# Kernel optimization log

Hardware: AMD Instinct MI355X
Metric: run time of the kernel (lower is better)

Reference implementation:

```python
import jax, jax.numpy as jnp
import numpy as np

CONF_THRESH = 0.3
NMS_THRESH = 0.5
TOP_K = 64
VAR = (0.1, 0.2)  # standard SSD decode variances


def setup_inputs() -> dict:
    key = jax.random.key(0)
    k1, k2, k3 = jax.random.split(key, 3)
    B, A, C = 16, 16384, 81
    loc = jax.random.normal(k1, (B, A, 4), jnp.float32)
    conf = jax.random.normal(k2, (B, A, C), jnp.float32)
    anchors = jax.random.uniform(k3, (A, 4), jnp.float32)  # cxcywh in [0,1]
    return {"loc": loc, "conf": conf, "anchors": anchors}


def _decode(loc, anchors):
    # SSD-style decode: loc [A,4] offsets, anchors [A,4] cxcywh -> corners [A,4]
    cxcy = anchors[:, :2] + loc[:, :2] * VAR[0] * anchors[:, 2:]
    wh = anchors[:, 2:] * jnp.exp(loc[:, 2:] * VAR[1])
    tl = cxcy - wh * 0.5
    return jnp.concatenate([tl, tl + wh], axis=1)


def _iou(box, boxes):
    # box [4], boxes [A,4] in corner format
    tl = jnp.maximum(box[:2], boxes[:, :2])
    br = jnp.minimum(box[2:], boxes[:, 2:])
    wh = jnp.clip(br - tl, 0.0)
    inter = wh[:, 0] * wh[:, 1]
    a1 = (box[2] - box[0]) * (box[3] - box[1])
    a2 = (boxes[:, 2] - boxes[:, 0]) * (boxes[:, 3] - boxes[:, 1])
    return inter / (a1 + a2 - inter)


def _nms(boxes, scores):
    # greedy NMS for one (batch, class) lane; boxes [A,4], scores [A]
    s0 = jnp.where(scores > CONF_THRESH, scores, -1.0)

    def step(s, _):
        i = jnp.argmax(s)
        sc = s[i]
        box = boxes[i]
        keep = sc > 0.0  # -1 means masked/suppressed; valid scores > conf_thresh > 0
        supp = jnp.where(_iou(box, boxes) > NMS_THRESH, -1.0, s).at[i].set(-1.0)
        s_next = jnp.where(keep, supp, s)
        row = jnp.where(keep, jnp.concatenate([sc[None], box]),
                        jnp.zeros((5,), s.dtype))
        return s_next, row

    _, rows = jax.lax.scan(step, s0, None, length=TOP_K)
    return rows  # [TOP_K, 5] = (score, x1, y1, x2, y2), zero-padded


def reference(loc, conf, anchors):
    conf = jax.nn.sigmoid(conf)                      # [B,A,C]
    boxes = jax.vmap(_decode, in_axes=(0, None))(loc, anchors)  # [B,A,4]
    scores = jnp.swapaxes(conf, 1, 2)                # [B,C,A]
    per_class = jax.vmap(_nms, in_axes=(None, 0))    # over classes
    out = jax.vmap(per_class)(boxes, scores)         # [B,C,TOP_K,5]
    return out
```

## Files before the change

kernel.cpp:

```cpp
#include <hip/hip_runtime.h>
#include <math.h>

constexpr int B_N  = 16;
constexpr int A_N  = 16384;
constexpr int C_N  = 81;
constexpr int TOPK = 64;
constexpr int DNT  = 256;
constexpr int NBINS = 232;
constexpr int CAP   = 512;
constexpr unsigned BIN_BASE = 0x3E99u;
constexpr int SNT = 256;
constexpr int BC_N = B_N * C_N;

constexpr int TA   = 64;
constexpr int TNT  = 256;
constexpr int TILE_ELEMS = TA * C_N;
constexpr int TILE_F4    = TILE_ELEMS / 4;

__global__ __launch_bounds__(DNT) void decode_kernel(const float4* __restrict__ loc,
                                                     const float4* __restrict__ anch,
                                                     float4* __restrict__ boxes) {
    int i = blockIdx.x * DNT + threadIdx.x;
    int a = i & (A_N - 1);
    float4 l  = loc[i];
    float4 an = anch[a];
    float cx = an.x + (l.x * 0.1f) * an.z;
    float cy = an.y + (l.y * 0.1f) * an.w;
    float w  = an.z * expf(l.z * 0.2f);
    float h  = an.w * expf(l.w * 0.2f);
    float x1 = cx - w * 0.5f;
    float y1 = cy - h * 0.5f;
    boxes[i] = make_float4(x1, y1, x1 + w, y1 + h);
}

__global__ __launch_bounds__(TNT) void sigT_kernel(const float* __restrict__ conf,
                                                   float* __restrict__ scoresT) {
    __shared__ float4 tile4[TILE_F4];
    float* tile = (float*)tile4;

    const int a0 = blockIdx.x * TA;
    const int b  = blockIdx.y;
    const int t  = threadIdx.x;

    const float4* src = (const float4*)(conf + ((size_t)b * A_N + a0) * C_N);
#pragma unroll
    for (int i = 0; i < (TILE_F4 + TNT - 1) / TNT; ++i) {
        int idx4 = i * TNT + t;
        if (idx4 < TILE_F4) {
            float4 x = src[idx4];
            float4 v;
            v.x = 1.0f / (1.0f + expf(-x.x));
            v.y = 1.0f / (1.0f + expf(-x.y));
            v.z = 1.0f / (1.0f + expf(-x.z));
            v.w = 1.0f / (1.0f + expf(-x.w));
            tile4[idx4] = v;
        }
    }
    __syncthreads();
    float* dst = scoresT + (size_t)b * C_N * A_N + a0;
#pragma unroll
    for (int i = 0; i < (TILE_F4 + TNT - 1) / TNT; ++i) {
        int idx4 = i * TNT + t;
        if (idx4 < TILE_F4) {
            int cc  = idx4 >> 4;
            int al4 = idx4 & 15;
            int e   = al4 * 4 * C_N + cc;
            float4 v;
            v.x = tile[e];
            v.y = tile[e + C_N];
            v.z = tile[e + 2 * C_N];
            v.w = tile[e + 3 * C_N];
            ((float4*)(dst + (size_t)cc * A_N))[al4] = v;
        }
    }
}

__device__ __forceinline__ void sort_gather_scan64(
        unsigned long long* cand, float4* cbox, int C, int lane,
        const float4* __restrict__ bptr, float* __restrict__ optr,
        float& rx1, float& ry1, float& rx2, float& ry2, float& rar,
        int& acc, int& kout) {
    unsigned long long key[8];
#pragma unroll
    for (int r = 0; r < 8; ++r) {
        int sidx = r * 64 + lane;
        key[r] = (sidx < C) ? cand[sidx] : 0ull;
    }
#pragma unroll
    for (int k = 2; k <= CAP; k <<= 1) {
#pragma unroll
        for (int j = k >> 1; j > 0; j >>= 1) {
            if (j >= 64) {
                int jr = j >> 6;
#pragma unroll
                for (int r = 0; r < 8; ++r) {
                    int rp = r ^ jr;
                    if (rp > r) {
                        int e = r * 64 + lane;
                        bool up = ((e & k) == 0);
                        unsigned long long va = key[r], vb = key[rp];
                        bool sw = up ? (va < vb) : (va > vb);
                        if (sw) { key[r] = vb; key[rp] = va; }
                    }
                }
            } else {
#pragma unroll
                for (int r = 0; r < 8; ++r) {
                    int e = r * 64 + lane;
                    bool up    = ((e & k) == 0);
                    bool isLow = ((lane & j) == 0);
                    unsigned long long va = key[r];
                    unsigned long long vb = __shfl_xor(va, j, 64);
                    bool keepMax = (up == isLow);
                    key[r] = keepMax ? (va > vb ? va : vb) : (va < vb ? va : vb);
                }
            }
        }
    }
    __syncthreads();
#pragma unroll
    for (int r = 0; r < 8; ++r) cand[r * 64 + lane] = key[r];
    __syncthreads();
#pragma unroll
    for (int r = 0; r < 8; ++r) {
        int e = r * 64 + lane;
        if (e < C) cbox[e] = bptr[(int)(~(unsigned)cand[e])];
    }
    __syncthreads();

    int ts = 0;
    unsigned long long k0 = cand[0];
    float4 cb = cbox[0];
    while (ts < C) {
        unsigned long long nk = 0ull;
        float4 nb = cb;
        if (ts + 1 < C) { nk = cand[ts + 1]; nb = cbox[ts + 1]; }
        float sc = __uint_as_float((unsigned)(k0 >> 32));
        float ca = (cb.z - cb.x) * (cb.w - cb.y);
        bool over = false;
        if (lane < acc) {
            float tlx = fmaxf(rx1, cb.x);
            float tly = fmaxf(ry1, cb.y);
            float brx = fminf(rx2, cb.z);
            float bry = fminf(ry2, cb.w);
            float iw  = fmaxf(brx - tlx, 0.0f);
            float ih  = fmaxf(bry - tly, 0.0f);
            float inter = iw * ih;
            float iou = inter / (rar + ca - inter);
            over = iou > 0.5f;
        }
        if (!__any(over)) {
            if (lane == acc) { rx1 = cb.x; ry1 = cb.y; rx2 = cb.z; ry2 = cb.w; rar = ca; }
            if (lane == 0) {
                float* o = optr + (size_t)kout * 5;
                o[0] = sc; o[1] = cb.x; o[2] = cb.y; o[3] = cb.z; o[4] = cb.w;
            }
            acc++; kout++;
            if (acc == TOPK) break;
        }
        ++ts; k0 = nk; cb = nb;
    }
}

__device__ __forceinline__ void suppress_pass(
        unsigned& aliveM, const float4& bb, float bar,
        const float4 (&breg)[8], const float (&careg)[8]) {
#pragma unroll
    for (int r = 0; r < 8; ++r) {
        float tlx = fmaxf(bb.x, breg[r].x);
        float tly = fmaxf(bb.y, breg[r].y);
        float brx = fminf(bb.z, breg[r].z);
        float bry = fminf(bb.w, breg[r].w);
        float iw  = fmaxf(brx - tlx, 0.0f);
        float ih  = fmaxf(bry - tly, 0.0f);
        float inter = iw * ih;
        float iou = inter / (bar + careg[r] - inter);
        if (iou > 0.5f) aliveM &= ~(1u << r);
    }
}

__device__ __forceinline__ void process_band64(
        unsigned long long* cand, float4* cbox, float4* abox, float* aar,
        int C, int lane,
        const float4* __restrict__ bptr, float* __restrict__ optr,
        int& acc, int& kout) {
    unsigned long long key[8];
#pragma unroll
    for (int r = 0; r < 8; ++r) {
        int sidx = r * 64 + lane;
        key[r] = (sidx < C) ? cand[sidx] : 0ull;
    }
#pragma unroll
    for (int k = 2; k <= CAP; k <<= 1) {
#pragma unroll
        for (int j = k >> 1; j > 0; j >>= 1) {
            if (j >= 64) {
                int jr = j >> 6;
#pragma unroll
                for (int r = 0; r < 8; ++r) {
                    int rp = r ^ jr;
                    if (rp > r) {
                        int e = r * 64 + lane;
                        bool up = ((e & k) == 0);
                        unsigned long long va = key[r], vb = key[rp];
                        bool sw = up ? (va < vb) : (va > vb);
                        if (sw) { key[r] = vb; key[rp] = va; }
                    }
                }
            } else {
#pragma unroll
                for (int r = 0; r < 8; ++r) {
                    int e = r * 64 + lane;
                    bool up    = ((e & k) == 0);
                    bool isLow = ((lane & j) == 0);
                    unsigned long long va = key[r];
                    unsigned long long vb = __shfl_xor(va, j, 64);
                    bool keepMax = (up == isLow);
                    key[r] = keepMax ? (va > vb ? va : vb) : (va < vb ? va : vb);
                }
            }
        }
    }
    __syncthreads();
#pragma unroll
    for (int r = 0; r < 8; ++r) cand[r * 64 + lane] = key[r];
    __syncthreads();

    float4 breg[8];
    float  careg[8];
#pragma unroll
    for (int r = 0; r < 8; ++r) {
        int e = r * 64 + lane;
        float4 v = make_float4(0.f, 0.f, 0.f, 0.f);
        if (e < C) { v = bptr[(int)(~(unsigned)cand[e])]; cbox[e] = v; }
        breg[r]  = v;
        careg[r] = (v.z - v.x) * (v.w - v.y);
    }
    __syncthreads();

    unsigned aliveM = 0;
#pragma unroll
    for (int r = 0; r < 8; ++r)
        if (r * 64 + lane < C) aliveM |= (1u << r);

    for (int a = 0; a < acc; ++a) {
        float4 bb = abox[a];
        float bar = aar[a];
        suppress_pass(aliveM, bb, bar, breg, careg);
    }

    int rStart = 0;
    while (acc < TOPK) {
        int estar = -1;
        for (int r = rStart; r < 8; ++r) {
            unsigned long long m = __ballot((aliveM >> r) & 1);
            if (m != 0ull) { estar = r * 64 + __builtin_ctzll(m); rStart = r; break; }
        }
        if (estar < 0) break;

        unsigned long long k0 = cand[estar];
        float4 bb = cbox[estar];
        float sc  = __uint_as_float((unsigned)(k0 >> 32));
        float bar = (bb.z - bb.x) * (bb.w - bb.y);

        if (lane == 0) {
            float* o = optr + (size_t)kout * 5;
            o[0] = sc; o[1] = bb.x; o[2] = bb.y; o[3] = bb.z; o[4] = bb.w;
            abox[acc] = bb; aar[acc] = bar;
        }
        acc++; kout++;

        suppress_pass(aliveM, bb, bar, breg, careg);
    }
}

__global__ __launch_bounds__(SNT) void select_kernel(
        const float* __restrict__ scoresT,
        unsigned long long* __restrict__ g_cand,
        int* __restrict__ g_hist,
        int* __restrict__ g_cnt,
        int* __restrict__ g_blo) {
    __shared__ int hist[NBINS];
    __shared__ int s_cnt;

    const int bc = blockIdx.x;
    const int t  = threadIdx.x;

    for (int i = t; i < NBINS; i += SNT) hist[i] = 0;
    if (t == 0) s_cnt = 0;
    __syncthreads();

    const float4* sptr = (const float4*)(scoresT + (size_t)bc * A_N);

    for (int i = 0; i < A_N / 4 / SNT; ++i) {
        float4 s4 = sptr[t + SNT * i];
        float s[4] = {s4.x, s4.y, s4.z, s4.w};
#pragma unroll
        for (int q = 0; q < 4; ++q) {
            if (s[q] > 0.3f) {
                unsigned u = __float_as_uint(s[q]);
                int bin = (int)(u >> 16) - (int)BIN_BASE;
                bin = bin < 0 ? 0 : (bin > NBINS - 1 ? NBINS - 1 : bin);
                atomicAdd(&hist[bin], 1);
            }
        }
    }
    __syncthreads();

    for (int i = t; i < NBINS; i += SNT) g_hist[bc * NBINS + i] = hist[i];

    int lo = NBINS, tot = 0;
    while (lo > 0) {
        int cnt = hist[lo - 1];
        if (tot + cnt > CAP) {
            if (tot == 0) { lo--; }
            break;
        }
        tot += cnt; lo--;
    }
    const int bin_lo = lo;

    if (bin_lo < NBINS) {
        for (int i = 0; i < A_N / 4 / SNT; ++i) {
            float4 s4 = sptr[t + SNT * i];
            float s[4] = {s4.x, s4.y, s4.z, s4.w};
#pragma unroll
            for (int q = 0; q < 4; ++q) {
                if (s[q] > 0.3f) {
                    unsigned u = __float_as_uint(s[q]);
                    int bin = (int)(u >> 16) - (int)BIN_BASE;
                    bin = bin < 0 ? 0 : (bin > NBINS - 1 ? NBINS - 1 : bin);
                    if (bin >= bin_lo && bin < NBINS) {
                        int slot = atomicAdd(&s_cnt, 1);
                        if (slot < CAP) {
                            unsigned a = (unsigned)(4 * (t + SNT * i) + q);
                            g_cand[(size_t)bc * CAP + slot] =
                                ((unsigned long long)u << 32) | (unsigned)(~a);
                        }
                    }
                }
            }
        }
    }
    __syncthreads();
    if (t == 0) {
        int C = s_cnt; if (C > CAP) C = CAP;
        g_cnt[bc] = C;
        g_blo[bc] = bin_lo;
    }
}

__global__ __launch_bounds__(64, 2) void nms_sorted_kernel(
        const float* __restrict__ scoresT,
        const float4* __restrict__ boxes,
        const unsigned long long* __restrict__ g_cand,
        const int* __restrict__ g_hist,
        const int* __restrict__ g_cnt,
        const int* __restrict__ g_blo,
        float* __restrict__ out) {
    __shared__ int hist[NBINS];
    __shared__ unsigned long long cand[CAP];
    __shared__ float4 cbox[CAP];
    __shared__ float4 abox[TOPK];
    __shared__ float  aar[TOPK];
    __shared__ int s_cnt;

    const int bc   = blockIdx.x;
    const int b    = bc / C_N;
    const int lane = threadIdx.x;

    const float4* sptr = (const float4*)(scoresT + (size_t)bc * A_N);
    const float4* bptr = boxes + (size_t)b * A_N;
    float* optr = out + (size_t)bc * TOPK * 5;

    for (int i = lane; i < NBINS; i += 64) hist[i] = g_hist[bc * NBINS + i];
    const int C0 = g_cnt[bc];
    int bin_hi   = g_blo[bc];
    for (int e = lane; e < C0; e += 64) cand[e] = g_cand[(size_t)bc * CAP + e];
    __syncthreads();

    int acc = 0, kout = 0;

    if (C0 > 0)
        process_band64(cand, cbox, abox, aar, C0, lane, bptr, optr, acc, kout);

    while (acc < TOPK) {
        int lo = bin_hi, tot = 0;
        while (lo > 0) {
            int cnt = hist[lo - 1];
            if (tot + cnt > CAP) {
                if (tot == 0) { lo--; }
                break;
            }
            tot += cnt; lo--;
        }
        const int bin_lo = lo;
        if (bin_lo == bin_hi) break;
        if (lane == 0) s_cnt = 0;
        __syncthreads();

        for (int i = 0; i < A_N / 4 / 64; ++i) {
            float4 s4 = sptr[lane + 64 * i];
            float s[4] = {s4.x, s4.y, s4.z, s4.w};
#pragma unroll
            for (int q = 0; q < 4; ++q) {
                if (s[q] > 0.3f) {
                    unsigned u = __float_as_uint(s[q]);
                    int bin = (int)(u >> 16) - (int)BIN_BASE;
                    bin = bin < 0 ? 0 : (bin > NBINS - 1 ? NBINS - 1 : bin);
                    if (bin >= bin_lo && bin < bin_hi) {
                        int slot = atomicAdd(&s_cnt, 1);
                        if (slot < CAP) {
                            unsigned a = (unsigned)(4 * (lane + 64 * i) + q);
                            cand[slot] = ((unsigned long long)u << 32) | (unsigned)(~a);
                        }
                    }
                }
            }
        }
        __syncthreads();
        int C = s_cnt; if (C > CAP) C = CAP;
        if (C > 0)
            process_band64(cand, cbox, abox, aar, C, lane, bptr, optr, acc, kout);
        bin_hi = bin_lo;
    }

    {
        float* o  = optr + (size_t)kout * 5;
        int   rem = (TOPK - kout) * 5;
        for (int i = lane; i < rem; i += 64) o[i] = 0.0f;
    }
}

__global__ __launch_bounds__(SNT, 4) void select_nms_fused(
        const float* __restrict__ scoresT,
        const float4* __restrict__ boxes,
        float* __restrict__ out) {
    __shared__ int hist[NBINS];
    __shared__ unsigned long long cand[CAP];
    __shared__ float4 cbox[CAP];
    __shared__ int s_cnt, s_acc, s_kout;

    const int bc   = blockIdx.x;
    const int b    = bc / C_N;
    const int t    = threadIdx.x;
    const int lane = t & 63;
    const int wv   = t >> 6;

    for (int i = t; i < NBINS; i += SNT) hist[i] = 0;
    if (t == 0) { s_acc = 0; s_kout = 0; }
    __syncthreads();

    const float4* sptr = (const float4*)(scoresT + (size_t)bc * A_N);
    const float4* bptr = boxes + (size_t)b * A_N;
    float* optr = out + (size_t)bc * TOPK * 5;

    for (int i = 0; i < A_N / 4 / SNT; ++i) {
        float4 s4 = sptr[t + SNT * i];
        float s[4] = {s4.x, s4.y, s4.z, s4.w};
#pragma unroll
        for (int q = 0; q < 4; ++q) {
            if (s[q] > 0.3f) {
                unsigned u = __float_as_uint(s[q]);
                int bin = (int)(u >> 16) - (int)BIN_BASE;
                bin = bin < 0 ? 0 : (bin > NBINS - 1 ? NBINS - 1 : bin);
                atomicAdd(&hist[bin], 1);
            }
        }
    }
    __syncthreads();

    float rx1 = 0.f, ry1 = 0.f, rx2 = 0.f, ry2 = 0.f, rar = 0.f;
    int acc = 0, kout = 0;

    int bin_hi = NBINS;
    for (;;) {
        int lo = bin_hi, tot = 0;
        while (lo > 0) {
            int cnt = hist[lo - 1];
            if (tot + cnt > CAP) { if (tot == 0) { lo--; } break; }
            tot += cnt; lo--;
        }
        const int bin_lo = lo;
        if (bin_lo == bin_hi) break;
        if (t == 0) s_cnt = 0;
        __syncthreads();

        for (int i = 0; i < A_N / 4 / SNT; ++i) {
            float4 s4 = sptr[t + SNT * i];
            float s[4] = {s4.x, s4.y, s4.z, s4.w};
#pragma unroll
            for (int q = 0; q < 4; ++q) {
                if (s[q] > 0.3f) {
                    unsigned u = __float_as_uint(s[q]);
                    int bin = (int)(u >> 16) - (int)BIN_BASE;
                    bin = bin < 0 ? 0 : (bin > NBINS - 1 ? NBINS - 1 : bin);
                    if (bin >= bin_lo && bin < bin_hi) {
                        int slot = atomicAdd(&s_cnt, 1);
                        if (slot < CAP) {
                            unsigned a = (unsigned)(4 * (t + SNT * i) + q);
                            cand[slot] = ((unsigned long long)u << 32) | (unsigned)(~a);
                        }
                    }
                }
            }
        }
        __syncthreads();
        int C = s_cnt; if (C > CAP) C = CAP;

        if (C > 0) {
            if (wv == 0) {
                unsigned long long key[8];
#pragma unroll
                for (int r = 0; r < 8; ++r) {
                    int sidx = r * 64 + lane;
                    key[r] = (sidx < C) ? cand[sidx] : 0ull;
                }
#pragma unroll
                for (int k = 2; k <= CAP; k <<= 1) {
#pragma unroll
                    for (int j = k >> 1; j > 0; j >>= 1) {
                        if (j >= 64) {
                            int jr = j >> 6;
#pragma unroll
                            for (int r = 0; r < 8; ++r) {
                                int rp = r ^ jr;
                                if (rp > r) {
                                    int e = r * 64 + lane;
                                    bool up = ((e & k) == 0);
                                    unsigned long long va = key[r], vb = key[rp];
                                    bool sw = up ? (va < vb) : (va > vb);
                                    if (sw) { key[r] = vb; key[rp] = va; }
                                }
                            }
                        } else {
#pragma unroll
                            for (int r = 0; r < 8; ++r) {
                                int e = r * 64 + lane;
                                bool up    = ((e & k) == 0);
                                bool isLow = ((lane & j) == 0);
                                unsigned long long va = key[r];
                                unsigned long long vb = __shfl_xor(va, j, 64);
                                bool keepMax = (up == isLow);
                                key[r] = keepMax ? (va > vb ? va : vb)
                                                 : (va < vb ? va : vb);
                            }
                        }
                    }
                }
#pragma unroll
                for (int r = 0; r < 8; ++r) cand[r * 64 + lane] = key[r];
            }
            __syncthreads();

            for (int e = t; e < CAP; e += SNT)
                if (e < C) cbox[e] = bptr[(int)(~(unsigned)cand[e])];
            __syncthreads();

            if (wv == 0) {
                int ts = 0;
                unsigned long long k0 = cand[0];
                float4 cb = cbox[0];
                while (ts < C) {
                    unsigned long long nk = 0ull;
                    float4 nb = cb;
                    if (ts + 1 < C) { nk = cand[ts + 1]; nb = cbox[ts + 1]; }
                    float sc = __uint_as_float((unsigned)(k0 >> 32));
                    float ca = (cb.z - cb.x) * (cb.w - cb.y);
                    bool over = false;
                    if (lane < acc) {
                        float tlx = fmaxf(rx1, cb.x);
                        float tly = fmaxf(ry1, cb.y);
                        float brx = fminf(rx2, cb.z);
                        float bry = fminf(ry2, cb.w);
                        float iw  = fmaxf(brx - tlx, 0.0f);
                        float ih  = fmaxf(bry - tly, 0.0f);
                        float inter = iw * ih;
                        float iou = inter / (rar + ca - inter);
                        over = iou > 0.5f;
                    }
                    if (!__any(over)) {
                        if (lane == acc) { rx1 = cb.x; ry1 = cb.y; rx2 = cb.z; ry2 = cb.w; rar = ca; }
                        if (lane == 0) {
                            float* o = optr + (size_t)kout * 5;
                            o[0] = sc; o[1] = cb.x; o[2] = cb.y; o[3] = cb.z; o[4] = cb.w;
                        }
                        acc++; kout++;
                        if (acc == TOPK) break;
                    }
                    ++ts; k0 = nk; cb = nb;
                }
                if (lane == 0) { s_acc = acc; s_kout = kout; }
            }
            __syncthreads();
            if (s_acc >= TOPK) break;
        }
        bin_hi = bin_lo;
    }

    {
        const int ko = s_kout;
        float* o  = optr + (size_t)ko * 5;
        int   rem = (TOPK - ko) * 5;
        for (int i = t; i < rem; i += SNT) o[i] = 0.0f;
    }
}

__global__ __launch_bounds__(64, 4) void nms_fallback(const float* __restrict__ conf,
                                                      const float4* __restrict__ boxes,
                                                      float* __restrict__ out) {
    __shared__ int hist[NBINS];
    __shared__ unsigned long long cand[CAP];
    __shared__ float4 cbox[CAP];
    __shared__ int s_cnt;

    const int c    = blockIdx.x;
    const int b    = blockIdx.y;
    const int lane = threadIdx.x;

    const float4* bptr = boxes + (size_t)b * A_N;
    const float*  cptr = conf + (size_t)b * A_N * C_N + c;
    float* optr = out + (size_t)(b * C_N + c) * TOPK * 5;

    for (int i = lane; i < NBINS; i += 64) hist[i] = 0;
    __syncthreads();
    for (int i = 0; i < A_N / 256; ++i) {
        int a0 = 4 * (lane + 64 * i);
#pragma unroll
        for (int q = 0; q < 4; ++q) {
            float x = cptr[(size_t)(a0 + q) * C_N];
            float s = 1.0f / (1.0f + expf(-x));
            if (s > 0.3f) {
                unsigned u = __float_as_uint(s);
                int bin = (int)(u >> 16) - (int)BIN_BASE;
                bin = bin < 0 ? 0 : (bin > NBINS - 1 ? NBINS - 1 : bin);
                atomicAdd(&hist[bin], 1);
            }
        }
    }
    __syncthreads();

    float rx1 = 0.f, ry1 = 0.f, rx2 = 0.f, ry2 = 0.f, rar = 0.f;
    int acc = 0, kout = 0;
    int bin_hi = NBINS;
    for (;;) {
        int lo = bin_hi, tot = 0;
        while (lo > 0) {
            int cnt = hist[lo - 1];
            if (tot + cnt > CAP) { if (tot == 0) { lo--; } break; }
            tot += cnt; lo--;
        }
        const int bin_lo = lo;
        if (bin_lo == bin_hi) break;
        if (lane == 0) s_cnt = 0;
        __syncthreads();
        for (int i = 0; i < A_N / 256; ++i) {
            int a0 = 4 * (lane + 64 * i);
#pragma unroll
            for (int q = 0; q < 4; ++q) {
                float x = cptr[(size_t)(a0 + q) * C_N];
                float s = 1.0f / (1.0f + expf(-x));
                if (s > 0.3f) {
                    unsigned u = __float_as_uint(s);
                    int bin = (int)(u >> 16) - (int)BIN_BASE;
                    bin = bin < 0 ? 0 : (bin > NBINS - 1 ? NBINS - 1 : bin);
                    if (bin >= bin_lo && bin < bin_hi) {
                        int slot = atomicAdd(&s_cnt, 1);
                        if (slot < CAP)
                            cand[slot] = ((unsigned long long)u << 32) | (unsigned)(~(unsigned)(a0 + q));
                    }
                }
            }
        }
        __syncthreads();
        int C = s_cnt; if (C > CAP) C = CAP;
        if (C > 0)
            sort_gather_scan64(cand, cbox, C, lane, bptr, optr,
                               rx1, ry1, rx2, ry2, rar, acc, kout);
        if (acc == TOPK) break;
        bin_hi = bin_lo;
    }
    {
        float* o  = optr + (size_t)kout * 5;
        int   rem = (TOPK - kout) * 5;
        for (int i = lane; i < rem; i += 64) o[i] = 0.0f;
    }
}

extern "C" void kernel_launch(void* const* d_in, const int* in_sizes, int n_in,
                              void* d_out, int out_size, void* d_ws, size_t ws_size,
                              hipStream_t stream) {
    const float* loc     = (const float*)d_in[0];
    const float* conf    = (const float*)d_in[1];
    const float* anchors = (const float*)d_in[2];
    float* out = (float*)d_out;

    const size_t boxes_bytes  = (size_t)B_N * A_N * sizeof(float4);
    const size_t scores_bytes = (size_t)B_N * C_N * A_N * sizeof(float);
    const size_t cand_bytes   = (size_t)BC_N * CAP * sizeof(unsigned long long);
    const size_t hist_bytes   = (size_t)BC_N * NBINS * sizeof(int);
    const size_t cnt_bytes    = (size_t)BC_N * sizeof(int);
    const size_t full_bytes   = boxes_bytes + scores_bytes + cand_bytes +
                                hist_bytes + 2 * cnt_bytes;

    float4* boxes = (float4*)d_ws;

    decode_kernel<<<(B_N * A_N) / DNT, DNT, 0, stream>>>(
        (const float4*)loc, (const float4*)anchors, boxes);

    if (ws_size >= full_bytes) {
        char* p = (char*)d_ws + boxes_bytes;
        float* scoresT = (float*)p;                 p += scores_bytes;
        unsigned long long* g_cand = (unsigned long long*)p; p += cand_bytes;
        int* g_hist = (int*)p;                      p += hist_bytes;
        int* g_cnt  = (int*)p;                      p += cnt_bytes;
        int* g_blo  = (int*)p;

        sigT_kernel<<<dim3(A_N / TA, B_N), TNT, 0, stream>>>(conf, scoresT);
        select_kernel<<<dim3(BC_N), SNT, 0, stream>>>(scoresT, g_cand, g_hist, g_cnt, g_blo);
        nms_sorted_kernel<<<dim3(BC_N), 64, 0, stream>>>(scoresT, boxes, g_cand,
                                                         g_hist, g_cnt, g_blo, out);
    } else if (ws_size >= boxes_bytes + scores_bytes) {
        float* scoresT = (float*)((char*)d_ws + boxes_bytes);
        sigT_kernel<<<dim3(A_N / TA, B_N), TNT, 0, stream>>>(conf, scoresT);
        select_nms_fused<<<dim3(BC_N), SNT, 0, stream>>>(scoresT, boxes, out);
    } else {
        nms_fallback<<<dim3(C_N, B_N), 64, 0, stream>>>(conf, boxes, out);
    }
}
```

Before: 254.8 us.

## Bucket candidates by score bin globally so NMS bands skip rescanning scores

The select kernel now builds a suffix sum over the score histogram and scatters every above-threshold candidate into a bin-ordered global buffer of up to GCAP_MAX entries per lane. The NMS kernel reads each band directly from that buffer instead of rescanning the 16K scores with atomics for every band after the first, and keeps the reading of candidates in registers before sorting. The IoU test also changes from a division to a double-precision multiply comparison. In exchange the select pass writes more candidates to global memory, and any band beyond the buffer capacity still uses the old rescan path.

```diff
diff --git a/kernel.cpp b/kernel.cpp
--- a/kernel.cpp
+++ b/kernel.cpp
@@ -11,6 +11,9 @@
 constexpr unsigned BIN_BASE = 0x3E99u;
 constexpr int SNT = 256;
 constexpr int BC_N = B_N * C_N;
+constexpr int GCAP_MAX = 2048;
+
+#define IOU_HALF_EXACT 0x1.000001p-1
 
 constexpr int TA   = 64;
 constexpr int TNT  = 256;
@@ -162,7 +165,7 @@
     }
 }
 
-__device__ __forceinline__ void suppress_pass(
+__device__ __forceinline__ void suppress_mask(
         unsigned& aliveM, const float4& bb, float bar,
         const float4 (&breg)[8], const float (&careg)[8]) {
 #pragma unroll
@@ -174,22 +177,16 @@
         float iw  = fmaxf(brx - tlx, 0.0f);
         float ih  = fmaxf(bry - tly, 0.0f);
         float inter = iw * ih;
-        float iou = inter / (bar + careg[r] - inter);
-        if (iou > 0.5f) aliveM &= ~(1u << r);
-    }
-}
-
-__device__ __forceinline__ void process_band64(
+        float den = bar + careg[r] - inter;
+        if ((double)inter > (double)den * IOU_HALF_EXACT) aliveM &= ~(1u << r);
+    }
+}
+
+__device__ __forceinline__ void sort_mask_accept(
+        unsigned long long (&key)[8], int C, int lane,
         unsigned long long* cand, float4* cbox, float4* abox, float* aar,
-        int C, int lane,
         const float4* __restrict__ bptr, float* __restrict__ optr,
         int& acc, int& kout) {
-    unsigned long long key[8];
-#pragma unroll
-    for (int r = 0; r < 8; ++r) {
-        int sidx = r * 64 + lane;
-        key[r] = (sidx < C) ? cand[sidx] : 0ull;
-    }
 #pragma unroll
     for (int k = 2; k <= CAP; k <<= 1) {
 #pragma unroll
@@ -232,7 +229,7 @@
     for (int r = 0; r < 8; ++r) {
         int e = r * 64 + lane;
         float4 v = make_float4(0.f, 0.f, 0.f, 0.f);
-        if (e < C) { v = bptr[(int)(~(unsigned)cand[e])]; cbox[e] = v; }
+        if (e < C) { v = bptr[(int)(~(unsigned)key[r])]; cbox[e] = v; }
         breg[r]  = v;
         careg[r] = (v.z - v.x) * (v.w - v.y);
     }
@@ -243,11 +240,8 @@
     for (int r = 0; r < 8; ++r)
         if (r * 64 + lane < C) aliveM |= (1u << r);
 
-    for (int a = 0; a < acc; ++a) {
-        float4 bb = abox[a];
-        float bar = aar[a];
-        suppress_pass(aliveM, bb, bar, breg, careg);
-    }
+    for (int a = 0; a < acc; ++a)
+        suppress_mask(aliveM, abox[a], aar[a], breg, careg);
 
     int rStart = 0;
     while (acc < TOPK) {
@@ -270,7 +264,7 @@
         }
         acc++; kout++;
 
-        suppress_pass(aliveM, bb, bar, breg, careg);
+        suppress_mask(aliveM, bb, bar, breg, careg);
     }
 }
 
@@ -278,16 +272,15 @@
         const float* __restrict__ scoresT,
         unsigned long long* __restrict__ g_cand,
         int* __restrict__ g_hist,
-        int* __restrict__ g_cnt,
-        int* __restrict__ g_blo) {
+        int gcap) {
     __shared__ int hist[NBINS];
-    __shared__ int s_cnt;
+    __shared__ int cur[NBINS];
+    __shared__ int sfx[NBINS + 1];
 
     const int bc = blockIdx.x;
     const int t  = threadIdx.x;
 
-    for (int i = t; i < NBINS; i += SNT) hist[i] = 0;
-    if (t == 0) s_cnt = 0;
+    for (int i = t; i < NBINS; i += SNT) { hist[i] = 0; cur[i] = 0; }
     __syncthreads();
 
     const float4* sptr = (const float4*)(scoresT + (size_t)bc * A_N);
@@ -308,57 +301,44 @@
     __syncthreads();
 
     for (int i = t; i < NBINS; i += SNT) g_hist[bc * NBINS + i] = hist[i];
-
-    int lo = NBINS, tot = 0;
-    while (lo > 0) {
-        int cnt = hist[lo - 1];
-        if (tot + cnt > CAP) {
-            if (tot == 0) { lo--; }
-            break;
-        }
-        tot += cnt; lo--;
-    }
-    const int bin_lo = lo;
-
-    if (bin_lo < NBINS) {
-        for (int i = 0; i < A_N / 4 / SNT; ++i) {
-            float4 s4 = sptr[t + SNT * i];
-            float s[4] = {s4.x, s4.y, s4.z, s4.w};
-#pragma unroll
-            for (int q = 0; q < 4; ++q) {
-                if (s[q] > 0.3f) {
-                    unsigned u = __float_as_uint(s[q]);
-                    int bin = (int)(u >> 16) - (int)BIN_BASE;
-                    bin = bin < 0 ? 0 : (bin > NBINS - 1 ? NBINS - 1 : bin);
-                    if (bin >= bin_lo && bin < NBINS) {
-                        int slot = atomicAdd(&s_cnt, 1);
-                        if (slot < CAP) {
-                            unsigned a = (unsigned)(4 * (t + SNT * i) + q);
-                            g_cand[(size_t)bc * CAP + slot] =
-                                ((unsigned long long)u << 32) | (unsigned)(~a);
-                        }
-                    }
-                }
-            }
-        }
-    }
-    __syncthreads();
     if (t == 0) {
-        int C = s_cnt; if (C > CAP) C = CAP;
-        g_cnt[bc] = C;
-        g_blo[bc] = bin_lo;
-    }
-}
-
-__global__ __launch_bounds__(64, 2) void nms_sorted_kernel(
+        sfx[NBINS] = 0;
+        for (int b = NBINS - 1; b >= 0; --b) sfx[b] = sfx[b + 1] + hist[b];
+    }
+    __syncthreads();
+
+    unsigned long long* gc = g_cand + (size_t)bc * gcap;
+    for (int i = 0; i < A_N / 4 / SNT; ++i) {
+        float4 s4 = sptr[t + SNT * i];
+        float s[4] = {s4.x, s4.y, s4.z, s4.w};
+#pragma unroll
+        for (int q = 0; q < 4; ++q) {
+            if (s[q] > 0.3f) {
+                unsigned u = __float_as_uint(s[q]);
+                int bin = (int)(u >> 16) - (int)BIN_BASE;
+                bin = bin < 0 ? 0 : (bin > NBINS - 1 ? NBINS - 1 : bin);
+                int base = sfx[bin + 1];
+                if (base < gcap) {
+                    int g = base + atomicAdd(&cur[bin], 1);
+                    if (g < gcap) {
+                        unsigned a = (unsigned)(4 * (t + SNT * i) + q);
+                        gc[g] = ((unsigned long long)u << 32) | (unsigned)(~a);
+                    }
+                }
+            }
+        }
+    }
+}
+
+__global__ __launch_bounds__(64, 2) void nms_banded_kernel(
         const float* __restrict__ scoresT,
         const float4* __restrict__ boxes,
         const unsigned long long* __restrict__ g_cand,
         const int* __restrict__ g_hist,
-        const int* __restrict__ g_cnt,
-        const int* __restrict__ g_blo,
-        float* __restrict__ out) {
+        float* __restrict__ out,
+        int gcap) {
     __shared__ int hist[NBINS];
+    __shared__ int sfx[NBINS + 1];
     __shared__ unsigned long long cand[CAP];
     __shared__ float4 cbox[CAP];
     __shared__ float4 abox[TOPK];
@@ -371,18 +351,19 @@
 
     const float4* sptr = (const float4*)(scoresT + (size_t)bc * A_N);
     const float4* bptr = boxes + (size_t)b * A_N;
+    const unsigned long long* gc = g_cand + (size_t)bc * gcap;
     float* optr = out + (size_t)bc * TOPK * 5;
 
     for (int i = lane; i < NBINS; i += 64) hist[i] = g_hist[bc * NBINS + i];
-    const int C0 = g_cnt[bc];
-    int bin_hi   = g_blo[bc];
-    for (int e = lane; e < C0; e += 64) cand[e] = g_cand[(size_t)bc * CAP + e];
+    __syncthreads();
+    if (lane == 0) {
+        sfx[NBINS] = 0;
+        for (int bn = NBINS - 1; bn >= 0; --bn) sfx[bn] = sfx[bn + 1] + hist[bn];
+    }
     __syncthreads();
 
     int acc = 0, kout = 0;
-
-    if (C0 > 0)
-        process_band64(cand, cbox, abox, aar, C0, lane, bptr, optr, acc, kout);
+    int bin_hi = NBINS;
 
     while (acc < TOPK) {
         int lo = bin_hi, tot = 0;
@@ -396,32 +377,57 @@
         }
         const int bin_lo = lo;
         if (bin_lo == bin_hi) break;
-        if (lane == 0) s_cnt = 0;
-        __syncthreads();
-
-        for (int i = 0; i < A_N / 4 / 64; ++i) {
-            float4 s4 = sptr[lane + 64 * i];
-            float s[4] = {s4.x, s4.y, s4.z, s4.w};
-#pragma unroll
-            for (int q = 0; q < 4; ++q) {
-                if (s[q] > 0.3f) {
-                    unsigned u = __float_as_uint(s[q]);
-                    int bin = (int)(u >> 16) - (int)BIN_BASE;
-                    bin = bin < 0 ? 0 : (bin > NBINS - 1 ? NBINS - 1 : bin);
-                    if (bin >= bin_lo && bin < bin_hi) {
-                        int slot = atomicAdd(&s_cnt, 1);
-                        if (slot < CAP) {
-                            unsigned a = (unsigned)(4 * (lane + 64 * i) + q);
-                            cand[slot] = ((unsigned long long)u << 32) | (unsigned)(~a);
+
+        const int start = sfx[bin_hi];
+        int C = sfx[bin_lo] - start;
+        if (C > CAP) C = CAP;
+
+        if (C > 0) {
+            if (start + C <= gcap) {
+                unsigned long long key[8];
+#pragma unroll
+                for (int r = 0; r < 8; ++r) {
+                    int e = r * 64 + lane;
+                    key[r] = (e < C) ? gc[start + e] : 0ull;
+                }
+                sort_mask_accept(key, C, lane, cand, cbox, abox, aar,
+                                 bptr, optr, acc, kout);
+            } else {
+                if (lane == 0) s_cnt = 0;
+                __syncthreads();
+                for (int i = 0; i < A_N / 4 / 64; ++i) {
+                    float4 s4 = sptr[lane + 64 * i];
+                    float s[4] = {s4.x, s4.y, s4.z, s4.w};
+#pragma unroll
+                    for (int q = 0; q < 4; ++q) {
+                        if (s[q] > 0.3f) {
+                            unsigned u = __float_as_uint(s[q]);
+                            int bin = (int)(u >> 16) - (int)BIN_BASE;
+                            bin = bin < 0 ? 0 : (bin > NBINS - 1 ? NBINS - 1 : bin);
+                            if (bin >= bin_lo && bin < bin_hi) {
+                                int slot = atomicAdd(&s_cnt, 1);
+                                if (slot < CAP) {
+                                    unsigned a = (unsigned)(4 * (lane + 64 * i) + q);
+                                    cand[slot] = ((unsigned long long)u << 32) | (unsigned)(~a);
+                                }
+                            }
                         }
                     }
                 }
-            }
-        }
-        __syncthreads();
-        int C = s_cnt; if (C > CAP) C = CAP;
-        if (C > 0)
-            process_band64(cand, cbox, abox, aar, C, lane, bptr, optr, acc, kout);
+                __syncthreads();
+                int Cr = s_cnt; if (Cr > CAP) Cr = CAP;
+                if (Cr > 0) {
+                    unsigned long long key[8];
+#pragma unroll
+                    for (int r = 0; r < 8; ++r) {
+                        int e = r * 64 + lane;
+                        key[r] = (e < Cr) ? cand[e] : 0ull;
+                    }
+                    sort_mask_accept(key, Cr, lane, cand, cbox, abox, aar,
+                                     bptr, optr, acc, kout);
+                }
+            }
+        }
         bin_hi = bin_lo;
     }
 
@@ -697,29 +703,29 @@
 
     const size_t boxes_bytes  = (size_t)B_N * A_N * sizeof(float4);
     const size_t scores_bytes = (size_t)B_N * C_N * A_N * sizeof(float);
-    const size_t cand_bytes   = (size_t)BC_N * CAP * sizeof(unsigned long long);
     const size_t hist_bytes   = (size_t)BC_N * NBINS * sizeof(int);
-    const size_t cnt_bytes    = (size_t)BC_N * sizeof(int);
-    const size_t full_bytes   = boxes_bytes + scores_bytes + cand_bytes +
-                                hist_bytes + 2 * cnt_bytes;
+    const size_t fixed_bytes  = boxes_bytes + scores_bytes + hist_bytes;
+    const size_t min_cand     = (size_t)BC_N * CAP * sizeof(unsigned long long);
 
     float4* boxes = (float4*)d_ws;
 
     decode_kernel<<<(B_N * A_N) / DNT, DNT, 0, stream>>>(
         (const float4*)loc, (const float4*)anchors, boxes);
 
-    if (ws_size >= full_bytes) {
+    if (ws_size >= fixed_bytes + min_cand) {
+        size_t avail = ws_size - fixed_bytes;
+        int gcap = (int)(avail / ((size_t)BC_N * sizeof(unsigned long long)));
+        if (gcap > GCAP_MAX) gcap = GCAP_MAX;
+
         char* p = (char*)d_ws + boxes_bytes;
         float* scoresT = (float*)p;                 p += scores_bytes;
-        unsigned long long* g_cand = (unsigned long long*)p; p += cand_bytes;
         int* g_hist = (int*)p;                      p += hist_bytes;
-        int* g_cnt  = (int*)p;                      p += cnt_bytes;
-        int* g_blo  = (int*)p;
+        unsigned long long* g_cand = (unsigned long long*)p;
 
         sigT_kernel<<<dim3(A_N / TA, B_N), TNT, 0, stream>>>(conf, scoresT);
-        select_kernel<<<dim3(BC_N), SNT, 0, stream>>>(scoresT, g_cand, g_hist, g_cnt, g_blo);
-        nms_sorted_kernel<<<dim3(BC_N), 64, 0, stream>>>(scoresT, boxes, g_cand,
-                                                         g_hist, g_cnt, g_blo, out);
+        select_kernel<<<dim3(BC_N), SNT, 0, stream>>>(scoresT, g_cand, g_hist, gcap);
+        nms_banded_kernel<<<dim3(BC_N), 64, 0, stream>>>(scoresT, boxes, g_cand,
+                                                         g_hist, out, gcap);
     } else if (ws_size >= boxes_bytes + scores_bytes) {
         float* scoresT = (float*)((char*)d_ws + boxes_bytes);
         sigT_kernel<<<dim3(A_N / TA, B_N), TNT, 0, stream>>>(conf, scoresT);
```

Result: slower. 268.3 us (+5.3%).
